# Optimization experiments

Hardware: AMD Instinct MI355X
Metric: run time of the kernel (lower is better)

The kernel has to match this reference:

```python
import math
import jax, jax.numpy as jnp
import numpy as np

DIM = 2048
HID = 4 * DIM
SEQ = 2048
BATCH = 2
EPS = 1e-5


def _layernorm(x, g, b):
    mu = jnp.mean(x, axis=-1, keepdims=True)
    var = jnp.var(x, axis=-1, keepdims=True)
    return (x - mu) * jax.lax.rsqrt(var + EPS) * g + b


def setup_inputs() -> dict:
    key = jax.random.key(0)
    ks = jax.random.split(key, 12)
    s = 1.0 / math.sqrt(DIM)
    x = jax.random.normal(ks[0], (BATCH, SEQ, DIM), dtype=jnp.float32)
    # additive causal mask: 0 on/below diagonal, -1e9 above
    mask = jnp.where(jnp.tril(jnp.ones((SEQ, SEQ), dtype=bool)), 0.0, -1e9).astype(jnp.float32)
    freqs_cis = jax.random.normal(ks[1], (SEQ, 64), dtype=jnp.float32)  # unused by forward
    return {
        "x": x,
        "mask": mask,
        "start_pos": 0,
        "freqs_cis": freqs_cis,
        "wq": jax.random.normal(ks[2], (DIM, DIM), dtype=jnp.float32) * s,
        "bq": jnp.zeros((DIM,), dtype=jnp.float32),
        "wk": jax.random.normal(ks[3], (DIM, DIM), dtype=jnp.float32) * s,
        "bk": jnp.zeros((DIM,), dtype=jnp.float32),
        "wv": jax.random.normal(ks[4], (DIM, DIM), dtype=jnp.float32) * s,
        "bv": jnp.zeros((DIM,), dtype=jnp.float32),
        "g_ln1": jnp.ones((DIM,), dtype=jnp.float32),
        "b_ln1": jnp.zeros((DIM,), dtype=jnp.float32),
        "g_ln2": jnp.ones((DIM,), dtype=jnp.float32),
        "b_ln2": jnp.zeros((DIM,), dtype=jnp.float32),
        "w1": jax.random.normal(ks[5], (DIM, HID), dtype=jnp.float32) * s,
        "b1": jnp.zeros((HID,), dtype=jnp.float32),
        "w2": jax.random.normal(ks[6], (HID, DIM), dtype=jnp.float32) * (1.0 / math.sqrt(HID)),
        "b2": jnp.zeros((DIM,), dtype=jnp.float32),
    }


def reference(x, mask, start_pos, freqs_cis, wq, bq, wk, bk, wv, bv,
              g_ln1, b_ln1, g_ln2, b_ln2, w1, b1, w2, b2):
    # pre-norm attention (no head split; scale by sqrt(full dim); dropout=eval identity)
    h = _layernorm(x, g_ln1, b_ln1)
    q = h @ wq + bq
    k = h @ wk + bk
    v = h @ wv + bv
    scores = jnp.einsum('bqd,bkd->bqk', q, k) / math.sqrt(DIM) + mask
    attn = jax.nn.softmax(scores, axis=-1)
    attn_out = jnp.einsum('bqk,bkd->bqd', attn, v)
    h2 = _layernorm(x + attn_out, g_ln2, b_ln2)
    ffn = jax.nn.gelu(h2 @ w1 + b1, approximate=False) @ w2 + b2
    # NOTE: original code adds FFN output to the ORIGINAL x (attn residual dropped here)
    return x + ffn
```

## Files before the change

kernel.cpp:

```cpp
#include <hip/hip_runtime.h>
#include <math.h>

#define DIM_ 2048
#define HID_ 8192
#define SEQ_ 2048
#define BATCH_ 2
#define TOK_ (BATCH_*SEQ_)

typedef __attribute__((ext_vector_type(4))) float f32x4;
typedef __attribute__((ext_vector_type(8))) __bf16 bf16x8;
typedef __attribute__((ext_vector_type(4))) unsigned int u32x4;
typedef __attribute__((ext_vector_type(4))) short s16x4;
typedef __attribute__((address_space(3))) short* lds_sp;

__device__ __forceinline__ short f2bf(float f) {
  union { float f; unsigned u; } v; v.f = f;
  unsigned r = v.u + 0x7FFFu + ((v.u >> 16) & 1u);
  return (short)(r >> 16);
}

__device__ __forceinline__ f32x4 mfma16(u32x4 a, u32x4 b, f32x4 c) {
  return __builtin_amdgcn_mfma_f32_16x16x32_bf16(
      __builtin_bit_cast(bf16x8, a), __builtin_bit_cast(bf16x8, b), c, 0, 0, 0);
}

#define DSR(dst, addr) asm volatile("ds_read_b128 %0, %1" : "=v"(dst) : "v"(addr))

#define RD_A(mlo, slot) do { \
  const unsigned ab_ = aBase + (unsigned)(slot)*16384u + (mlo)*2048u; \
  DSR(af[0][0], ab_ + offk0);         DSR(af[0][1], ab_ + offk1); \
  DSR(af[1][0], ab_ + 2048u + offk0); DSR(af[1][1], ab_ + 2048u + offk1); \
} while(0)

#define RD_B(slot) do { \
  const unsigned bb_ = bBase + (unsigned)(slot)*32768u; \
  DSR(bfr[0][0], bb_ + offk0);         DSR(bfr[0][1], bb_ + offk1); \
  DSR(bfr[1][0], bb_ + 2048u + offk0); DSR(bfr[1][1], bb_ + 2048u + offk1); \
  DSR(bfr[2][0], bb_ + 4096u + offk0); DSR(bfr[2][1], bb_ + 4096u + offk1); \
  DSR(bfr[3][0], bb_ + 6144u + offk0); DSR(bfr[3][1], bb_ + 6144u + offk1); \
} while(0)

#define MM(mlo) do { \
  _Pragma("unroll") \
  for (int n_ = 0; n_ < 4; ++n_) { \
    acc[(mlo)][n_]   = mfma16(af[0][0], bfr[n_][0], acc[(mlo)][n_]); \
    acc[(mlo)][n_]   = mfma16(af[0][1], bfr[n_][1], acc[(mlo)][n_]); \
    acc[(mlo)+1][n_] = mfma16(af[1][0], bfr[n_][0], acc[(mlo)+1][n_]); \
    acc[(mlo)+1][n_] = mfma16(af[1][1], bfr[n_][1], acc[(mlo)+1][n_]); \
  } \
} while(0)

#define BARv()  __builtin_amdgcn_s_barrier()
#define LGKM0() do { asm volatile("s_waitcnt lgkmcnt(0)" ::: "memory"); \
                     __builtin_amdgcn_sched_barrier(0); } while(0)
#define LGKM8() asm volatile("s_waitcnt lgkmcnt(8)" ::: "memory")
#define VM6()   asm volatile("s_waitcnt vmcnt(6)" ::: "memory")

template<int EPI>
__global__ __launch_bounds__(512, 2)
void gemm8p(const short* __restrict__ A, const short* __restrict__ B,
            void* __restrict__ Cv, const float* __restrict__ bias,
            const float* __restrict__ aux,
            int M, int N, int K, int lda, int ldb, int ldc,
            long long sA, long long sB, long long sC)
{
  __shared__ __align__(16) short As[3*128*64];
  __shared__ __align__(16) short Bs[3*256*64];
  const int lane = threadIdx.x & 63;
  const int wave = threadIdx.x >> 6;
  const int wr = wave >> 2, wc = wave & 3;
  const int nwg  = gridDim.x * gridDim.y;
  const int orig = blockIdx.y * gridDim.x + blockIdx.x;
  const int wgid = (orig & 7) * (nwg >> 3) + (orig >> 3);
  const int tn = (wgid % gridDim.x) * 256;
  const int tm = (wgid / gridDim.x) * 128;
  const int z  = blockIdx.z;
  A += (long long)z * sA;
  B += (long long)z * sB;

  const int NT = K >> 6;

  const int lr    = lane >> 3;
  const int lrow  = wave * 8 + lr;
  const int lslot = ((lane & 7) ^ lr) << 3;
  const short* pA = A + (long long)(tm + lrow) * lda + lslot;
  const short* pB = B + (long long)(tn + lrow) * ldb + lslot;
  const long long lda64 = 64LL * lda;
  const long long ldb64 = 64LL * ldb;

  auto stageA = [&](int t, int slot) {
    const long long ko = (long long)t << 6;
    const int db = slot * 8192 + wave * 512;
    __builtin_amdgcn_global_load_lds(
        (const __attribute__((address_space(1))) void*)(pA + ko),
        (__attribute__((address_space(3))) void*)(As + db), 16, 0, 0);
    __builtin_amdgcn_global_load_lds(
        (const __attribute__((address_space(1))) void*)(pA + lda64 + ko),
        (__attribute__((address_space(3))) void*)(As + db + 4096), 16, 0, 0);
  };
  auto stageB = [&](int t, int slot) {
    const long long ko = (long long)t << 6;
    const int db = slot * 16384 + wave * 512;
    __builtin_amdgcn_global_load_lds(
        (const __attribute__((address_space(1))) void*)(pB + ko),
        (__attribute__((address_space(3))) void*)(Bs + db), 16, 0, 0);
    __builtin_amdgcn_global_load_lds(
        (const __attribute__((address_space(1))) void*)(pB + ldb64 + ko),
        (__attribute__((address_space(3))) void*)(Bs + db + 4096), 16, 0, 0);
    __builtin_amdgcn_global_load_lds(
        (const __attribute__((address_space(1))) void*)(pB + 2*ldb64 + ko),
        (__attribute__((address_space(3))) void*)(Bs + db + 8192), 16, 0, 0);
    __builtin_amdgcn_global_load_lds(
        (const __attribute__((address_space(1))) void*)(pB + 3*ldb64 + ko),
        (__attribute__((address_space(3))) void*)(Bs + db + 12288), 16, 0, 0);
  };

  const unsigned asB = (unsigned)(unsigned long long)(lds_sp)As;
  const unsigned bsB = (unsigned)(unsigned long long)(lds_sp)Bs;
  const int l15 = lane & 15, l4 = lane >> 4;
  const unsigned offk0 = (unsigned)(( l4      ^ (lane & 7)) << 4);
  const unsigned offk1 = (unsigned)(((l4 + 4) ^ (lane & 7)) << 4);
  const unsigned aBase = asB + (unsigned)((wr * 64 + l15) * 128);
  const unsigned bBase = bsB + (unsigned)((wc * 64 + l15) * 128);

  f32x4 acc[4][4] = {};
  u32x4 af[2][2], bfr[4][2];

  stageB(0, 0); stageA(0, 0);
  stageB(1 < NT ? 1 : 0, 1); stageA(1 < NT ? 1 : 0, 1);
  VM6();
  BARv();

  int rd = 0;
  #pragma unroll 1
  for (int t = 0; t < NT; ++t) {
    const int st = rd + 2 >= 3 ? rd - 1 : rd + 2;
    const int tc = t + 2 < NT ? t + 2 : NT - 1;
    RD_A(0, rd); RD_B(rd);
    stageB(tc, st);
    LGKM8();
    BARv(); LGKM0();
    __builtin_amdgcn_s_setprio(1); MM(0); __builtin_amdgcn_s_setprio(0);
    BARv();
    RD_A(2, rd);
    stageA(tc, st);
    VM6();
    BARv(); LGKM0();
    __builtin_amdgcn_s_setprio(1); MM(2); __builtin_amdgcn_s_setprio(0);
    BARv();
    rd = rd + 1 >= 3 ? 0 : rd + 1;
  }

  const int row0 = tm + wr * 64 + l4 * 4;
  const int col0 = tn + wc * 64 + l15;
  #pragma unroll
  for (int mi = 0; mi < 4; ++mi) {
    #pragma unroll
    for (int j = 0; j < 4; ++j) {
      const int row = row0 + mi * 16 + j;
      #pragma unroll
      for (int ni = 0; ni < 4; ++ni) {
        const int col = col0 + ni * 16;
        float v = acc[mi][ni][j];
        if (EPI == 1) {
          ((float*)Cv + (long long)z * sC)[(long long)row * ldc + col] = v;
        } else if (EPI == 0) {
          v += bias[col];
          ((short*)Cv + (long long)z * sC)[(long long)row * ldc + col] = f2bf(v);
        } else if (EPI == 2) {
          v += bias[col];
          v = 0.5f * v * (1.0f + erff(v * 0.70710678118654752f));
          ((short*)Cv + (long long)z * sC)[(long long)row * ldc + col] = f2bf(v);
        } else {
          v += bias[col] + aux[(long long)row * ldc + col];
          ((float*)Cv + (long long)z * sC)[(long long)row * ldc + col] = v;
        }
      }
    }
  }
}

__global__ __launch_bounds__(256)
void ln_kernel(const float* __restrict__ x, const float* __restrict__ res,
               const float* __restrict__ g, const float* __restrict__ b,
               short* __restrict__ out, int hasres)
{
  const int row = blockIdx.x;
  const int tid = threadIdx.x;
  const float4* X = (const float4*)x + (long long)row * 512;
  float4 v0 = X[tid], v1 = X[tid + 256];
  if (hasres) {
    const float4* R = (const float4*)res + (long long)row * 512;
    float4 r0 = R[tid], r1 = R[tid + 256];
    v0.x += r0.x; v0.y += r0.y; v0.z += r0.z; v0.w += r0.w;
    v1.x += r1.x; v1.y += r1.y; v1.z += r1.z; v1.w += r1.w;
  }
  float s1 = v0.x + v0.y + v0.z + v0.w + v1.x + v1.y + v1.z + v1.w;
  float s2 = v0.x*v0.x + v0.y*v0.y + v0.z*v0.z + v0.w*v0.w
           + v1.x*v1.x + v1.y*v1.y + v1.z*v1.z + v1.w*v1.w;
  #pragma unroll
  for (int o = 32; o > 0; o >>= 1) { s1 += __shfl_xor(s1, o); s2 += __shfl_xor(s2, o); }
  __shared__ float red[8];
  if ((tid & 63) == 0) { red[tid >> 6] = s1; red[4 + (tid >> 6)] = s2; }
  __syncthreads();
  s1 = red[0] + red[1] + red[2] + red[3];
  s2 = red[4] + red[5] + red[6] + red[7];
  const float mean = s1 * (1.0f / 2048.0f);
  const float var  = s2 * (1.0f / 2048.0f) - mean * mean;
  const float rstd = rsqrtf(var + 1e-5f);
  const float4* G  = (const float4*)g;
  const float4* Bb = (const float4*)b;
  float4 g0 = G[tid], g1 = G[tid + 256], b0 = Bb[tid], b1 = Bb[tid + 256];
  s16x4 o0, o1;
  o0[0] = f2bf((v0.x - mean) * rstd * g0.x + b0.x);
  o0[1] = f2bf((v0.y - mean) * rstd * g0.y + b0.y);
  o0[2] = f2bf((v0.z - mean) * rstd * g0.z + b0.z);
  o0[3] = f2bf((v0.w - mean) * rstd * g0.w + b0.w);
  o1[0] = f2bf((v1.x - mean) * rstd * g1.x + b1.x);
  o1[1] = f2bf((v1.y - mean) * rstd * g1.y + b1.y);
  o1[2] = f2bf((v1.z - mean) * rstd * g1.z + b1.z);
  o1[3] = f2bf((v1.w - mean) * rstd * g1.w + b1.w);
  *(s16x4*)&out[(long long)row * 2048 + tid * 4]        = o0;
  *(s16x4*)&out[(long long)row * 2048 + 1024 + tid * 4] = o1;
}

__global__ __launch_bounds__(256)
void softmax_kernel(const float* __restrict__ scores, const float* __restrict__ mask,
                    short* __restrict__ probs)
{
  const long long row = blockIdx.x;
  const int q  = blockIdx.x & (SEQ_ - 1);
  const int tid = threadIdx.x;
  const float scale = 0.022097086912079608f;
  const float4* S  = (const float4*)scores + row * 512;
  const float4* Mk = (const float4*)mask + (long long)q * 512;
  float4 v0 = S[tid], v1 = S[tid + 256];
  float4 m0 = Mk[tid], m1 = Mk[tid + 256];
  float a[8] = { v0.x*scale + m0.x, v0.y*scale + m0.y, v0.z*scale + m0.z, v0.w*scale + m0.w,
                 v1.x*scale + m1.x, v1.y*scale + m1.y, v1.z*scale + m1.z, v1.w*scale + m1.w };
  float mx = a[0];
  #pragma unroll
  for (int i = 1; i < 8; ++i) mx = fmaxf(mx, a[i]);
  #pragma unroll
  for (int o = 32; o > 0; o >>= 1) mx = fmaxf(mx, __shfl_xor(mx, o));
  __shared__ float red[8];
  if ((tid & 63) == 0) red[tid >> 6] = mx;
  __syncthreads();
  mx = fmaxf(fmaxf(red[0], red[1]), fmaxf(red[2], red[3]));
  float e[8], sum = 0.f;
  #pragma unroll
  for (int i = 0; i < 8; ++i) { e[i] = __expf(a[i] - mx); sum += e[i]; }
  #pragma unroll
  for (int o = 32; o > 0; o >>= 1) sum += __shfl_xor(sum, o);
  if ((tid & 63) == 0) red[4 + (tid >> 6)] = sum;
  __syncthreads();
  sum = red[4] + red[5] + red[6] + red[7];
  const float inv = 1.0f / sum;
  s16x4 o0, o1;
  #pragma unroll
  for (int i = 0; i < 4; ++i) o0[i] = f2bf(e[i] * inv);
  #pragma unroll
  for (int i = 0; i < 4; ++i) o1[i] = f2bf(e[4 + i] * inv);
  probs += row * 2048;
  *(s16x4*)&probs[tid * 4]        = o0;
  *(s16x4*)&probs[1024 + tid * 4] = o1;
}

__global__ __launch_bounds__(256)
void cvt_transpose_kernel(const float* __restrict__ in, short* __restrict__ out,
                          int R, int C)
{
  __shared__ float t[32][33];
  const int tx = threadIdx.x & 31, ty = threadIdx.x >> 5;
  const int r0 = blockIdx.y << 5, c0 = blockIdx.x << 5;
  #pragma unroll
  for (int i = 0; i < 32; i += 8)
    t[ty + i][tx] = in[(long long)(r0 + ty + i) * C + c0 + tx];
  __syncthreads();
  #pragma unroll
  for (int i = 0; i < 32; i += 8)
    out[(long long)(c0 + ty + i) * R + r0 + tx] = f2bf(t[tx][ty + i]);
}

__global__ __launch_bounds__(256)
void transpose_bf16_kernel(const short* __restrict__ in, short* __restrict__ out,
                           int ldin, int ldout, long long sin_, long long sout_)
{
  __shared__ short t[32][33];
  in  += (long long)blockIdx.z * sin_;
  out += (long long)blockIdx.z * sout_;
  const int tx = threadIdx.x & 31, ty = threadIdx.x >> 5;
  const int r0 = blockIdx.y << 5, c0 = blockIdx.x << 5;
  #pragma unroll
  for (int i = 0; i < 32; i += 8)
    t[ty + i][tx] = in[(long long)(r0 + ty + i) * ldin + c0 + tx];
  __syncthreads();
  #pragma unroll
  for (int i = 0; i < 32; i += 8)
    out[(long long)(c0 + ty + i) * ldout + r0 + tx] = t[tx][ty + i];
}

__global__ __launch_bounds__(256)
void concat_bias_kernel(const float* a, const float* b, const float* c, float* o)
{
  const int i = blockIdx.x * 256 + threadIdx.x;
  o[i] = i < 2048 ? a[i] : (i < 4096 ? b[i - 2048] : c[i - 4096]);
}

extern "C" void kernel_launch(void* const* d_in, const int* in_sizes, int n_in,
                              void* d_out, int out_size, void* d_ws, size_t ws_size,
                              hipStream_t stream)
{
  const float* x    = (const float*)d_in[0];
  const float* mask = (const float*)d_in[1];
  const float* wq   = (const float*)d_in[4];
  const float* bq   = (const float*)d_in[5];
  const float* wk   = (const float*)d_in[6];
  const float* bk   = (const float*)d_in[7];
  const float* wv   = (const float*)d_in[8];
  const float* bv   = (const float*)d_in[9];
  const float* g1   = (const float*)d_in[10];
  const float* b1   = (const float*)d_in[11];
  const float* g2   = (const float*)d_in[12];
  const float* b2   = (const float*)d_in[13];
  const float* w1   = (const float*)d_in[14];
  const float* bw1  = (const float*)d_in[15];
  const float* w2   = (const float*)d_in[16];
  const float* bw2  = (const float*)d_in[17];
  float* out = (float*)d_out;

  char* p = (char*)d_ws;
  auto take = [&](size_t bytes) { char* r = p; p += (bytes + 255) & ~(size_t)255; return r; };
  short* wqkvT = (short*)take((size_t)3 * DIM_ * DIM_ * 2);
  short* w1T   = (short*)take((size_t)DIM_ * HID_ * 2);
  short* w2T   = (short*)take((size_t)HID_ * DIM_ * 2);
  short* h_bf  = (short*)take((size_t)TOK_ * DIM_ * 2);
  short* qkv   = (short*)take((size_t)TOK_ * 3 * DIM_ * 2);
  short* vT    = (short*)take((size_t)BATCH_ * DIM_ * SEQ_ * 2);
  float* scores= (float*)take((size_t)BATCH_ * SEQ_ * SEQ_ * 4);
  short* attn  = (short*)take((size_t)BATCH_ * SEQ_ * SEQ_ * 2);
  float* cbias = (float*)take((size_t)3 * DIM_ * 4);
  short* ffn1  = qkv;
  float* attno = scores;
  short* h2    = h_bf;

  const dim3 blk(256), gblk(512);
  cvt_transpose_kernel<<<dim3(DIM_/32, DIM_/32), blk, 0, stream>>>(wq, wqkvT, DIM_, DIM_);
  cvt_transpose_kernel<<<dim3(DIM_/32, DIM_/32), blk, 0, stream>>>(wk, wqkvT + (size_t)DIM_*DIM_, DIM_, DIM_);
  cvt_transpose_kernel<<<dim3(DIM_/32, DIM_/32), blk, 0, stream>>>(wv, wqkvT + (size_t)2*DIM_*DIM_, DIM_, DIM_);
  cvt_transpose_kernel<<<dim3(HID_/32, DIM_/32), blk, 0, stream>>>(w1, w1T, DIM_, HID_);
  cvt_transpose_kernel<<<dim3(DIM_/32, HID_/32), blk, 0, stream>>>(w2, w2T, HID_, DIM_);
  concat_bias_kernel<<<24, blk, 0, stream>>>(bq, bk, bv, cbias);
  ln_kernel<<<TOK_, blk, 0, stream>>>(x, nullptr, g1, b1, h_bf, 0);
  gemm8p<0><<<dim3(6144/256, TOK_/128, 1), gblk, 0, stream>>>(
      h_bf, wqkvT, qkv, cbias, nullptr, TOK_, 6144, DIM_, DIM_, DIM_, 6144, 0, 0, 0);
  gemm8p<1><<<dim3(SEQ_/256, SEQ_/128, BATCH_), gblk, 0, stream>>>(
      qkv, qkv + DIM_, scores, nullptr, nullptr, SEQ_, SEQ_, DIM_, 6144, 6144, SEQ_,
      (long long)SEQ_ * 6144, (long long)SEQ_ * 6144, (long long)SEQ_ * SEQ_);
  softmax_kernel<<<BATCH_ * SEQ_, blk, 0, stream>>>(scores, mask, attn);
  transpose_bf16_kernel<<<dim3(DIM_/32, SEQ_/32, BATCH_), blk, 0, stream>>>(
      qkv + 2*DIM_, vT, 6144, SEQ_, (long long)SEQ_ * 6144, (long long)DIM_ * SEQ_);
  gemm8p<1><<<dim3(DIM_/256, SEQ_/128, BATCH_), gblk, 0, stream>>>(
      attn, vT, attno, nullptr, nullptr, SEQ_, DIM_, SEQ_, SEQ_, SEQ_, DIM_,
      (long long)SEQ_ * SEQ_, (long long)DIM_ * SEQ_, (long long)SEQ_ * DIM_);
  ln_kernel<<<TOK_, blk, 0, stream>>>(x, attno, g2, b2, h2, 1);
  gemm8p<2><<<dim3(HID_/256, TOK_/128, 1), gblk, 0, stream>>>(
      h2, w1T, ffn1, bw1, nullptr, TOK_, HID_, DIM_, DIM_, DIM_, HID_, 0, 0, 0);
  gemm8p<3><<<dim3(DIM_/256, TOK_/128, 1), gblk, 0, stream>>>(
      ffn1, w2T, out, bw2, x, TOK_, DIM_, HID_, HID_, HID_, DIM_, 0, 0, 0);
}
```

Before: 641.6 us.

## Add 256x256-tile GEMM with quadrant-split pipeline for QKV and FFN1

Adds a new GEMM kernel that computes 256x256 output tiles per workgroup, with each wave owning 128x64 and an 8-phase loop that double-buffers A and B and interleaves LDS reads, global-to-LDS loads and MFMA quadrants. The QKV projection and the first FFN GEMM now use it, which raises arithmetic intensity and cuts global and LDS traffic per FLOP compared with the 128x256 tiles. The tile-to-workgroup mapping also changes to group four N-tiles together for L2 locality, and this applies to the existing kernel too. In exchange, register pressure roughly doubles the accumulator count, which could cause spills at 2 waves per SIMD, and the larger tiles leave fewer workgroups per GEMM.

```diff
diff --git a/kernel.cpp b/kernel.cpp
--- a/kernel.cpp
+++ b/kernel.cpp
@@ -25,15 +25,195 @@
 }
 
 #define DSR(dst, addr) asm volatile("ds_read_b128 %0, %1" : "=v"(dst) : "v"(addr))
+#define BARv()  __builtin_amdgcn_s_barrier()
+#define LGKM0() do { asm volatile("s_waitcnt lgkmcnt(0)" ::: "memory"); \
+                     __builtin_amdgcn_sched_barrier(0); } while(0)
+#define LGKM8() asm volatile("s_waitcnt lgkmcnt(8)" ::: "memory")
+#define VM6()   asm volatile("s_waitcnt vmcnt(6)" ::: "memory")
+#define VM4()   asm volatile("s_waitcnt vmcnt(4)" ::: "memory")
+#define PRIO1() __builtin_amdgcn_s_setprio(1)
+#define PRIO0() __builtin_amdgcn_s_setprio(0)
+
+#define TILE_MAP(BM, BN) \
+  const int nwg  = gridDim.x * gridDim.y; \
+  const int orig = blockIdx.y * gridDim.x + blockIdx.x; \
+  const int wgid = (orig & 7) * (nwg >> 3) + (orig >> 3); \
+  const int gy4  = (int)gridDim.y << 2; \
+  const int rem  = wgid % gy4; \
+  const int tn   = ((wgid / gy4) * 4 + (rem & 3)) * (BN); \
+  const int tm   = (rem >> 2) * (BM);
+
+#define RA(mh, bufofs) do { \
+  _Pragma("unroll") \
+  for (int f_ = 0; f_ < 4; ++f_) { \
+    DSR(af[f_][0], aBase + (bufofs) + ((mh)*4+f_)*2048u + offk0); \
+    DSR(af[f_][1], aBase + (bufofs) + ((mh)*4+f_)*2048u + offk1); \
+  } \
+} while(0)
+
+#define RB(nh, bufofs) do { \
+  DSR(bq[nh][0][0], bBase + (bufofs) + (nh)*4096u + offk0); \
+  DSR(bq[nh][0][1], bBase + (bufofs) + (nh)*4096u + offk1); \
+  DSR(bq[nh][1][0], bBase + (bufofs) + (nh)*4096u + 2048u + offk0); \
+  DSR(bq[nh][1][1], bBase + (bufofs) + (nh)*4096u + 2048u + offk1); \
+} while(0)
+
+#define MMQ(mh, nh) do { \
+  _Pragma("unroll") \
+  for (int f_ = 0; f_ < 4; ++f_) { \
+    _Pragma("unroll") \
+    for (int c_ = 0; c_ < 2; ++c_) { \
+      acc[(mh)*4+f_][(nh)*2+c_] = mfma16(af[f_][0], bq[nh][c_][0], acc[(mh)*4+f_][(nh)*2+c_]); \
+      acc[(mh)*4+f_][(nh)*2+c_] = mfma16(af[f_][1], bq[nh][c_][1], acc[(mh)*4+f_][(nh)*2+c_]); \
+    } \
+  } \
+} while(0)
+
+template<int EPI>
+__global__ __launch_bounds__(512, 2)
+void gemm256(const short* __restrict__ A, const short* __restrict__ B,
+             void* __restrict__ Cv, const float* __restrict__ bias,
+             const float* __restrict__ aux,
+             int M, int N, int K, int lda, int ldb, int ldc,
+             long long sA, long long sB, long long sC)
+{
+  __shared__ __align__(16) short As[4*128*64];
+  __shared__ __align__(16) short Bs[4*128*64];
+  const int lane = threadIdx.x & 63;
+  const int wave = threadIdx.x >> 6;
+  const int wr = wave >> 2, wc = wave & 3;
+  TILE_MAP(256, 256)
+  const int z = blockIdx.z;
+  A += (long long)z * sA;
+  B += (long long)z * sB;
+
+  const int NT = K >> 6;
+  const int NI = NT >> 1;
+
+  const int lr    = lane >> 3;
+  const int lrow8 = wave * 8 + lr;
+  const int swz   = ((lane & 7) ^ lr) << 3;
+  const short* pA0 = A + (long long)(tm + lrow8) * lda + swz;
+  const short* pA1 = pA0 + 128LL * lda;
+  const short* pB0 = B + (long long)(tn + lrow8) * ldb + swz;
+  const short* pB1 = pB0 + 128LL * ldb;
+
+  auto stA = [&](const short* p, int t, int reg) {
+    const short* s = p + ((long long)t << 6);
+    __builtin_amdgcn_global_load_lds(
+        (const __attribute__((address_space(1))) void*)s,
+        (__attribute__((address_space(3))) void*)(As + reg + wave * 512), 16, 0, 0);
+    __builtin_amdgcn_global_load_lds(
+        (const __attribute__((address_space(1))) void*)(s + ((long long)lda << 6)),
+        (__attribute__((address_space(3))) void*)(As + reg + 4096 + wave * 512), 16, 0, 0);
+  };
+  auto stB = [&](const short* p, int t, int reg) {
+    const short* s = p + ((long long)t << 6);
+    __builtin_amdgcn_global_load_lds(
+        (const __attribute__((address_space(1))) void*)s,
+        (__attribute__((address_space(3))) void*)(Bs + reg + wave * 512), 16, 0, 0);
+    __builtin_amdgcn_global_load_lds(
+        (const __attribute__((address_space(1))) void*)(s + ((long long)ldb << 6)),
+        (__attribute__((address_space(3))) void*)(Bs + reg + 4096 + wave * 512), 16, 0, 0);
+  };
+
+  const unsigned asB = (unsigned)(unsigned long long)(lds_sp)As;
+  const unsigned bsB = (unsigned)(unsigned long long)(lds_sp)Bs;
+  const int l15 = lane & 15, l4 = lane >> 4;
+  const unsigned offk0 = (unsigned)(( l4      ^ (lane & 7)) << 4);
+  const unsigned offk1 = (unsigned)(((l4 + 4) ^ (lane & 7)) << 4);
+  const unsigned aBase = asB + (unsigned)(wr * 16384 + l15 * 128);
+  const unsigned bBase = bsB + (unsigned)((wc >> 1) * 16384 + (wc & 1) * 8192 + l15 * 128);
+
+  f32x4 acc[8][4] = {};
+  u32x4 af[4][2], bq[2][2][2];
+
+  stA(pA0, 0, 0);     stA(pA1, 0, 8192);
+  stB(pB0, 0, 0);     stB(pB1, 0, 8192);
+  stB(pB0, 1, 16384); stB(pB1, 1, 24576);
+  VM4(); BARv();
+
+  #pragma unroll 1
+  for (int i = 0; i < NI; ++i) {
+    const int t   = 2 * i;
+    const int tA  = t + 1;
+    const int t2  = t + 2 < NT ? t + 2 : NT - 1;
+    const int t3  = t + 3 < NT ? t + 3 : NT - 1;
+    RA(0, 0u); RB(0, 0u);
+    stA(pA0, tA, 16384);
+    LGKM8(); BARv(); LGKM0();
+    PRIO1(); MMQ(0, 0); PRIO0(); BARv();
+
+    RB(1, 0u);
+    stA(pA1, tA, 24576);
+    BARv(); LGKM0();
+    PRIO1(); MMQ(0, 1); PRIO0(); BARv();
+
+    RA(1, 0u);
+    stB(pB0, t2, 0);
+    BARv(); LGKM0();
+    PRIO1(); MMQ(1, 0); PRIO0(); BARv();
+
+    stB(pB1, t2, 8192);
+    VM4(); BARv();
+    PRIO1(); MMQ(1, 1); PRIO0(); BARv();
+    RA(0, 32768u); RB(0, 32768u);
+    stA(pA0, t2, 0);
+    LGKM8(); BARv(); LGKM0();
+    PRIO1(); MMQ(0, 0); PRIO0(); BARv();
+
+    RB(1, 32768u);
+    stA(pA1, t2, 8192);
+    BARv(); LGKM0();
+    PRIO1(); MMQ(0, 1); PRIO0(); BARv();
+
+    RA(1, 32768u);
+    stB(pB0, t3, 16384);
+    BARv(); LGKM0();
+    PRIO1(); MMQ(1, 0); PRIO0(); BARv();
+
+    stB(pB1, t3, 24576);
+    VM4(); BARv();
+    PRIO1(); MMQ(1, 1); PRIO0(); BARv();
+  }
+
+  const int row0 = tm + wr * 128 + l4 * 4;
+  const int col0 = tn + wc * 64 + l15;
+  #pragma unroll
+  for (int fr = 0; fr < 8; ++fr) {
+    #pragma unroll
+    for (int j = 0; j < 4; ++j) {
+      const int row = row0 + fr * 16 + j;
+      #pragma unroll
+      for (int fc = 0; fc < 4; ++fc) {
+        const int col = col0 + fc * 16;
+        float v = acc[fr][fc][j];
+        if (EPI == 1) {
+          ((float*)Cv + (long long)z * sC)[(long long)row * ldc + col] = v;
+        } else if (EPI == 0) {
+          v += bias[col];
+          ((short*)Cv + (long long)z * sC)[(long long)row * ldc + col] = f2bf(v);
+        } else if (EPI == 2) {
+          v += bias[col];
+          v = 0.5f * v * (1.0f + erff(v * 0.70710678118654752f));
+          ((short*)Cv + (long long)z * sC)[(long long)row * ldc + col] = f2bf(v);
+        } else {
+          v += bias[col] + aux[(long long)row * ldc + col];
+          ((float*)Cv + (long long)z * sC)[(long long)row * ldc + col] = v;
+        }
+      }
+    }
+  }
+}
 
 #define RD_A(mlo, slot) do { \
-  const unsigned ab_ = aBase + (unsigned)(slot)*16384u + (mlo)*2048u; \
+  const unsigned ab_ = aBase8 + (unsigned)(slot)*16384u + (mlo)*2048u; \
   DSR(af[0][0], ab_ + offk0);         DSR(af[0][1], ab_ + offk1); \
   DSR(af[1][0], ab_ + 2048u + offk0); DSR(af[1][1], ab_ + 2048u + offk1); \
 } while(0)
 
 #define RD_B(slot) do { \
-  const unsigned bb_ = bBase + (unsigned)(slot)*32768u; \
+  const unsigned bb_ = bBase8 + (unsigned)(slot)*32768u; \
   DSR(bfr[0][0], bb_ + offk0);         DSR(bfr[0][1], bb_ + offk1); \
   DSR(bfr[1][0], bb_ + 2048u + offk0); DSR(bfr[1][1], bb_ + 2048u + offk1); \
   DSR(bfr[2][0], bb_ + 4096u + offk0); DSR(bfr[2][1], bb_ + 4096u + offk1); \
@@ -50,12 +230,6 @@
   } \
 } while(0)
 
-#define BARv()  __builtin_amdgcn_s_barrier()
-#define LGKM0() do { asm volatile("s_waitcnt lgkmcnt(0)" ::: "memory"); \
-                     __builtin_amdgcn_sched_barrier(0); } while(0)
-#define LGKM8() asm volatile("s_waitcnt lgkmcnt(8)" ::: "memory")
-#define VM6()   asm volatile("s_waitcnt vmcnt(6)" ::: "memory")
-
 template<int EPI>
 __global__ __launch_bounds__(512, 2)
 void gemm8p(const short* __restrict__ A, const short* __restrict__ B,
@@ -69,11 +243,7 @@
   const int lane = threadIdx.x & 63;
   const int wave = threadIdx.x >> 6;
   const int wr = wave >> 2, wc = wave & 3;
-  const int nwg  = gridDim.x * gridDim.y;
-  const int orig = blockIdx.y * gridDim.x + blockIdx.x;
-  const int wgid = (orig & 7) * (nwg >> 3) + (orig >> 3);
-  const int tn = (wgid % gridDim.x) * 256;
-  const int tm = (wgid / gridDim.x) * 128;
+  TILE_MAP(128, 256)
   const int z  = blockIdx.z;
   A += (long long)z * sA;
   B += (long long)z * sB;
@@ -120,8 +290,8 @@
   const int l15 = lane & 15, l4 = lane >> 4;
   const unsigned offk0 = (unsigned)(( l4      ^ (lane & 7)) << 4);
   const unsigned offk1 = (unsigned)(((l4 + 4) ^ (lane & 7)) << 4);
-  const unsigned aBase = asB + (unsigned)((wr * 64 + l15) * 128);
-  const unsigned bBase = bsB + (unsigned)((wc * 64 + l15) * 128);
+  const unsigned aBase8 = asB + (unsigned)((wr * 64 + l15) * 128);
+  const unsigned bBase8 = bsB + (unsigned)((wc * 64 + l15) * 128);
 
   f32x4 acc[4][4] = {};
   u32x4 af[2][2], bfr[4][2];
@@ -140,13 +310,13 @@
     stageB(tc, st);
     LGKM8();
     BARv(); LGKM0();
-    __builtin_amdgcn_s_setprio(1); MM(0); __builtin_amdgcn_s_setprio(0);
+    PRIO1(); MM(0); PRIO0();
     BARv();
     RD_A(2, rd);
     stageA(tc, st);
     VM6();
     BARv(); LGKM0();
-    __builtin_amdgcn_s_setprio(1); MM(2); __builtin_amdgcn_s_setprio(0);
+    PRIO1(); MM(2); PRIO0();
     BARv();
     rd = rd + 1 >= 3 ? 0 : rd + 1;
   }
@@ -352,7 +522,7 @@
   cvt_transpose_kernel<<<dim3(DIM_/32, HID_/32), blk, 0, stream>>>(w2, w2T, HID_, DIM_);
   concat_bias_kernel<<<24, blk, 0, stream>>>(bq, bk, bv, cbias);
   ln_kernel<<<TOK_, blk, 0, stream>>>(x, nullptr, g1, b1, h_bf, 0);
-  gemm8p<0><<<dim3(6144/256, TOK_/128, 1), gblk, 0, stream>>>(
+  gemm256<0><<<dim3(6144/256, TOK_/256, 1), gblk, 0, stream>>>(
       h_bf, wqkvT, qkv, cbias, nullptr, TOK_, 6144, DIM_, DIM_, DIM_, 6144, 0, 0, 0);
   gemm8p<1><<<dim3(SEQ_/256, SEQ_/128, BATCH_), gblk, 0, stream>>>(
       qkv, qkv + DIM_, scores, nullptr, nullptr, SEQ_, SEQ_, DIM_, 6144, 6144, SEQ_,
@@ -364,7 +534,7 @@
       attn, vT, attno, nullptr, nullptr, SEQ_, DIM_, SEQ_, SEQ_, SEQ_, DIM_,
       (long long)SEQ_ * SEQ_, (long long)DIM_ * SEQ_, (long long)SEQ_ * DIM_);
   ln_kernel<<<TOK_, blk, 0, stream>>>(x, attno, g2, b2, h2, 1);
-  gemm8p<2><<<dim3(HID_/256, TOK_/128, 1), gblk, 0, stream>>>(
+  gemm256<2><<<dim3(HID_/256, TOK_/256, 1), gblk, 0, stream>>>(
       h2, w1T, ffn1, bw1, nullptr, TOK_, HID_, DIM_, DIM_, DIM_, HID_, 0, 0, 0);
   gemm8p<3><<<dim3(DIM_/256, TOK_/128, 1), gblk, 0, stream>>>(
       ffn1, w2T, out, bw2, x, TOK_, DIM_, HID_, HID_, HID_, DIM_, 0, 0, 0);
```

Result: slower. 684.0 us (+6.6%).
